# Kernel tuning notes

Measured on AMD Instinct MI355X. Metric: run time of the kernel, lower is better.

## Reference

```python
import math
import jax, jax.numpy as jnp
import numpy as np

B, S, DM, H, KH = 2, 2048, 1024, 16, 4
HD = DM // H          # 64
N_REP = H // KH       # 4
ROPE_THETA = 10000.0


def setup_inputs() -> dict:
    key = jax.random.key(0)
    ks = jax.random.split(key, 5)
    x = jax.random.normal(ks[0], (B, S, DM), dtype=jnp.float32)
    wq = jax.random.normal(ks[1], (H * HD, DM), dtype=jnp.float32) * 0.02
    wk = jax.random.normal(ks[2], (KH * HD, DM), dtype=jnp.float32) * 0.02
    wv = jax.random.normal(ks[3], (KH * HD, DM), dtype=jnp.float32) * 0.02
    wo = jax.random.normal(ks[4], (DM, H * HD), dtype=jnp.float32) * 0.02
    # freqs_cis = exp(i * t * theta^(-2j/d)) represented as cos/sin, shape [S, HD//2]
    inv_freq = 1.0 / (ROPE_THETA ** (jnp.arange(0, HD, 2, dtype=jnp.float32) / HD))
    angles = jnp.arange(S, dtype=jnp.float32)[:, None] * inv_freq[None, :]
    return {
        'x': x, 'wq': wq, 'wk': wk, 'wv': wv, 'wo': wo,
        'freqs_cos': jnp.cos(angles), 'freqs_sin': jnp.sin(angles),
    }


def _rope(t, cos, sin):
    # t: [B, S, h, HD]; pairs (even, odd) rotated as complex mul
    tr = t.reshape(*t.shape[:-1], HD // 2, 2)
    xr, xi = tr[..., 0], tr[..., 1]
    c = cos[None, :, None, :]  # [1, S, 1, HD//2]
    s = sin[None, :, None, :]
    out = jnp.stack([xr * c - xi * s, xr * s + xi * c], axis=-1)
    return out.reshape(t.shape)


def reference(x, wq, wk, wv, wo, freqs_cos, freqs_sin):
    b, s, _ = x.shape
    xq = (x @ wq.T).reshape(b, s, H, HD)
    xk = (x @ wk.T).reshape(b, s, KH, HD)
    xv = (x @ wv.T).reshape(b, s, KH, HD)
    xq = _rope(xq, freqs_cos, freqs_sin)
    xk = _rope(xk, freqs_cos, freqs_sin)
    # [B, h, S, HD]
    xq = xq.transpose(0, 2, 1, 3)
    xk = xk.transpose(0, 2, 1, 3)
    xv = xv.transpose(0, 2, 1, 3)
    # GQA: repeat_interleave kv heads to match query heads
    xk = jnp.repeat(xk, N_REP, axis=1)
    xv = jnp.repeat(xv, N_REP, axis=1)
    scale = 1.0 / math.sqrt(HD)
    scores = jnp.einsum('bhqd,bhkd->bhqk', xq, xk) * scale
    causal = jnp.tril(jnp.ones((s, s), dtype=bool))
    scores = jnp.where(causal[None, None], scores, jnp.finfo(scores.dtype).min)
    attn = jax.nn.softmax(scores, axis=-1)
    out = jnp.einsum('bhqk,bhkd->bhqd', attn, xv)
    out = out.transpose(0, 2, 1, 3).reshape(b, s, H * HD)
    return out @ wo.T
```

## Files before the change

### kernel.cpp

```cpp
#include <hip/hip_runtime.h>
#include <hip/hip_bf16.h>
#include <type_traits>

#define B_ 2
#define S_ 2048
#define DM_ 1024
#define H_ 16
#define KH_ 4
#define HD_ 64
#define NREP_ 4
#define QKV_LD 1536
#define CLOG 0.1803368801111244f
#define FIXM 8.0f

typedef float f32x4 __attribute__((ext_vector_type(4)));
typedef float f32x16 __attribute__((ext_vector_type(16)));
typedef short s16x8 __attribute__((ext_vector_type(8)));
typedef unsigned int u32x2 __attribute__((ext_vector_type(2)));

static __device__ __forceinline__ float bf2f(unsigned short u) {
  union { unsigned int u; float f; } x; x.u = ((unsigned int)u) << 16; return x.f;
}
static __device__ __forceinline__ unsigned short f2bf(float f) {
  union { float f; unsigned int u; } x; x.f = f;
  unsigned int r = (x.u + 0x7fffu + ((x.u >> 16) & 1u)) >> 16;
  return (unsigned short)r;
}
static __device__ __forceinline__ unsigned int cvtpk_bf16(float lo, float hi) {
  unsigned int r;
  asm("v_cvt_pk_bf16_f32 %0, %1, %2" : "=v"(r) : "v"(lo), "v"(hi));
  return r;
}
static __device__ __forceinline__ float fexp2(float x) {
  float r;
  asm("v_exp_f32 %0, %1" : "=v"(r) : "v"(x));
  return r;
}

__device__ __forceinline__ void gload_lds16(const unsigned short* g, unsigned short* l) {
  __builtin_amdgcn_global_load_lds(
      (const __attribute__((address_space(1))) unsigned int*)g,
      (__attribute__((address_space(3))) unsigned int*)l, 16, 0, 0);
}

__global__ void cvt_all_k(const float* __restrict__ x,
                          const float* __restrict__ wq, const float* __restrict__ wk,
                          const float* __restrict__ wv, const float* __restrict__ wo,
                          unsigned short* __restrict__ xb,
                          unsigned short* __restrict__ wqkv, unsigned short* __restrict__ wob) {
  int i = (blockIdx.x * 256 + threadIdx.x) * 4;
  const float* src; unsigned short* dst; int off;
  if (i < 4194304)      { src = x;  dst = xb;              off = i; }
  else if (i < 5242880) { src = wq; dst = wqkv;            off = i - 4194304; }
  else if (i < 5505024) { src = wk; dst = wqkv + 1048576;  off = i - 5242880; }
  else if (i < 5767168) { src = wv; dst = wqkv + 1310720;  off = i - 5505024; }
  else                  { src = wo; dst = wob;             off = i - 5767168; }
  float4 v = *(const float4*)(src + off);
  ushort4 o;
  o.x = f2bf(v.x); o.y = f2bf(v.y); o.z = f2bf(v.z); o.w = f2bf(v.w);
  *(ushort4*)(dst + off) = o;
}

#define BM 128
#define BN 128
#define BK 32

template <typename OT>
__global__ __launch_bounds__(512) void gemm_bt(const unsigned short* __restrict__ A,
                                               const unsigned short* __restrict__ Bw,
                                               OT* __restrict__ C,
                                               int M, int N, int K) {
  __shared__ unsigned short lds_a[BM * BK];
  __shared__ unsigned short lds_b[BN * BK];
  const int tid = threadIdx.x;
  const int wave = tid >> 6, lane = tid & 63;
  const int lr = lane & 15, lg = lane >> 4;
  const int m0 = blockIdx.y * BM, n0 = blockIdx.x * BN;
  const int wr = wave >> 2, wc = wave & 3;

  f32x4 acc[4][2] = {};

  const int srow = tid >> 2, scol = (tid & 3) << 3;

  for (int k0 = 0; k0 < K; k0 += BK) {
    gload_lds16(A + (size_t)(m0 + srow) * K + k0 + scol, &lds_a[tid * 8]);
    gload_lds16(Bw + (size_t)(n0 + srow) * K + k0 + scol, &lds_b[tid * 8]);
    __syncthreads();
    s16x8 af[4], bfr[2];
    #pragma unroll
    for (int mi = 0; mi < 4; ++mi)
      af[mi] = *(const s16x8*)&lds_a[(wr * 64 + mi * 16 + lr) * BK + lg * 8];
    #pragma unroll
    for (int ni = 0; ni < 2; ++ni)
      bfr[ni] = *(const s16x8*)&lds_b[(wc * 32 + ni * 16 + lr) * BK + lg * 8];
    #pragma unroll
    for (int mi = 0; mi < 4; ++mi) {
      #pragma unroll
      for (int ni = 0; ni < 2; ++ni)
        acc[mi][ni] = __builtin_amdgcn_mfma_f32_16x16x32_bf16(af[mi], bfr[ni], acc[mi][ni], 0, 0, 0);
    }
    __syncthreads();
  }
  #pragma unroll
  for (int mi = 0; mi < 4; ++mi) {
    #pragma unroll
    for (int ni = 0; ni < 2; ++ni) {
      #pragma unroll
      for (int r = 0; r < 4; ++r) {
        int row = m0 + wr * 64 + mi * 16 + lg * 4 + r;
        int col = n0 + wc * 32 + ni * 16 + lr;
        if constexpr (std::is_same<OT, unsigned short>::value)
          C[(size_t)row * N + col] = f2bf(acc[mi][ni][r]);
        else
          C[(size_t)row * N + col] = acc[mi][ni][r];
      }
    }
  }
}

__global__ void kvpack_k(const unsigned short* __restrict__ qkv,
                         const float* __restrict__ fc, const float* __restrict__ fs,
                         unsigned short* __restrict__ kp, unsigned short* __restrict__ vp) {
  int idx = blockIdx.x * 256 + threadIdx.x;
  int lane = idx & 63;
  int f  = (idx >> 6) & 3;
  int t  = (idx >> 8) & 63;
  int p  = idx >> 14;
  int b = p >> 2, kh = p & 3;
  int ql = lane & 31, hi = lane >> 5;
  {
    int s = t * 32 + ql;
    int d0 = f * 16 + hi * 8;
    const unsigned short* src = qkv + (size_t)(b * S_ + s) * QKV_LD + 1024 + kh * HD_ + d0;
    s16x8 v = *(const s16x8*)src;
    int i0 = d0 >> 1;
    float4 c4 = *(const float4*)(fc + s * 32 + i0);
    float4 s4 = *(const float4*)(fs + s * 32 + i0);
    float cc[4] = {c4.x, c4.y, c4.z, c4.w};
    float ss[4] = {s4.x, s4.y, s4.z, s4.w};
    union { s16x8 v; unsigned int w[4]; } o;
    #pragma unroll
    for (int e = 0; e < 4; ++e) {
      float xr = bf2f((unsigned short)v[2 * e]);
      float xi = bf2f((unsigned short)v[2 * e + 1]);
      o.w[e] = cvtpk_bf16(xr * cc[e] - xi * ss[e], xr * ss[e] + xi * cc[e]);
    }
    *(s16x8*)(kp + (size_t)idx * 8) = o.v;
  }
  {
    int d = (f >> 1) * 32 + ql;
    int kv0 = t * 32 + (f & 1) * 16 + hi * 8;
    const unsigned short* src = qkv + (size_t)(b * S_ + kv0) * QKV_LD + 1280 + kh * HD_ + d;
    s16x8 o;
    #pragma unroll
    for (int e = 0; e < 8; ++e) o[e] = (short)src[(size_t)e * QKV_LD];
    *(s16x8*)(vp + (size_t)idx * 8) = o;
  }
}

__global__ __launch_bounds__(256, 3) void attn_fwd10(const unsigned short* __restrict__ qkv,
                                                     const unsigned short* __restrict__ kp,
                                                     const unsigned short* __restrict__ vp,
                                                     const float* __restrict__ fc,
                                                     const float* __restrict__ fs,
                                                     unsigned short* __restrict__ ob) {
  __shared__ float mbuf[2][64][34];
  const int tid = threadIdx.x;
  const int wave = tid >> 6, lane = tid & 63;
  const int ql = lane & 31;
  const int hi = lane >> 5;
  const int bi = blockIdx.x;
  const int xcd = bi & 7;
  const int b = xcd >> 2, kh = xcd & 3;
  const int j = bi >> 3;
  const int h = kh * NREP_ + (j & 3);
  const int bt = j >> 2;

  int c, t0, t1;
  int sW1buf = -1, sM1buf = -1;
  bool sW2 = false, sM2 = false, doOut;
  if (bt < 32) {
    c = 63 - bt;
    int T = c + 1;
    t0 = (wave * T) >> 2; t1 = ((wave + 1) * T) >> 2;
    sW1buf = (wave == 1) ? 0 : (wave == 3) ? 1 : -1;
    sM1buf = (wave == 0) ? 0 : (wave == 2) ? 1 : -1;
    sW2 = (wave == 2); sM2 = (wave == 0);
    doOut = (wave == 0);
  } else if (bt < 40) {
    int bb2 = bt - 32;
    c = (wave < 2) ? (16 + bb2) : (31 - bb2);
    int T = c + 1, Th = T >> 1;
    if ((wave & 1) == 0) { t0 = 0;  t1 = Th; } else { t0 = Th; t1 = T; }
    sW1buf = (wave == 1) ? 0 : (wave == 3) ? 1 : -1;
    sM1buf = (wave == 0) ? 0 : (wave == 2) ? 1 : -1;
    doOut = (wave == 0) || (wave == 2);
  } else {
    c = (bt - 40) * 4 + wave;
    t0 = 0; t1 = c + 1;
    doOut = true;
  }
  const int q = c * 32 + ql;

  const unsigned short* qrow = qkv + (size_t)(b * S_ + q) * QKV_LD + h * HD_;
  s16x8 qf[4];
  #pragma unroll
  for (int ks = 0; ks < 4; ++ks) {
    s16x8 v = *(const s16x8*)(qrow + ks * 16 + hi * 8);
    int i0 = ks * 8 + hi * 4;
    float4 c4 = *(const float4*)(fc + q * 32 + i0);
    float4 s4 = *(const float4*)(fs + q * 32 + i0);
    float cc[4] = {c4.x, c4.y, c4.z, c4.w};
    float ss[4] = {s4.x, s4.y, s4.z, s4.w};
    union { s16x8 v; unsigned int w[4]; } o;
    #pragma unroll
    for (int e = 0; e < 4; ++e) {
      float xr = bf2f((unsigned short)v[2 * e]);
      float xi = bf2f((unsigned short)v[2 * e + 1]);
      o.w[e] = cvtpk_bf16(xr * cc[e] - xi * ss[e], xr * ss[e] + xi * cc[e]);
    }
    qf[ks] = o.v;
  }

  const unsigned short* kpt = kp + ((size_t)(b * KH_ + kh) << 17) + lane * 8;
  const unsigned short* vpt = vp + ((size_t)(b * KH_ + kh) << 17) + lane * 8;

  f32x16 oT0 = {};
  f32x16 oT1 = {};
  float l = 0.f;

  s16x8 ka[4], va[4], kb2[4], vb2[4];

#define LOADKV(T, KK, VV) do { \
    const unsigned short* kp_ = kpt + ((size_t)(T) << 11); \
    KK[0] = *(const s16x8*)(kp_);        KK[1] = *(const s16x8*)(kp_ + 512); \
    KK[2] = *(const s16x8*)(kp_ + 1024); KK[3] = *(const s16x8*)(kp_ + 1536); \
    const unsigned short* vp_ = vpt + ((size_t)(T) << 11); \
    VV[0] = *(const s16x8*)(vp_);        VV[1] = *(const s16x8*)(vp_ + 512); \
    VV[2] = *(const s16x8*)(vp_ + 1024); VV[3] = *(const s16x8*)(vp_ + 1536); \
  } while (0)

  auto body = [&](s16x8 (&KK)[4], s16x8 (&VV)[4], bool diag) __attribute__((always_inline)) {
    f32x16 st = {};
    __builtin_amdgcn_s_setprio(1);
    st = __builtin_amdgcn_mfma_f32_32x32x16_bf16(KK[0], qf[0], st, 0, 0, 0);
    st = __builtin_amdgcn_mfma_f32_32x32x16_bf16(KK[1], qf[1], st, 0, 0, 0);
    st = __builtin_amdgcn_mfma_f32_32x32x16_bf16(KK[2], qf[2], st, 0, 0, 0);
    st = __builtin_amdgcn_mfma_f32_32x32x16_bf16(KK[3], qf[3], st, 0, 0, 0);
    __builtin_amdgcn_s_setprio(0);
    if (diag) {
      #pragma unroll
      for (int r = 0; r < 16; ++r)
        if (((r & 3) + 8 * (r >> 2) + 4 * hi) > ql) st[r] = -1e30f;
    }
    float pr[16];
    #pragma unroll
    for (int r = 0; r < 16; ++r) pr[r] = fexp2(fmaf(st[r], CLOG, -FIXM));
    float s0 = (pr[0] + pr[1]) + (pr[2] + pr[3]);
    float s1 = (pr[4] + pr[5]) + (pr[6] + pr[7]);
    float s2 = (pr[8] + pr[9]) + (pr[10] + pr[11]);
    float s3 = (pr[12] + pr[13]) + (pr[14] + pr[15]);
    l += (s0 + s1) + (s2 + s3);
    #pragma unroll
    for (int ksv = 0; ksv < 2; ++ksv) {
      unsigned int a01 = cvtpk_bf16(pr[ksv * 8 + 0], pr[ksv * 8 + 1]);
      unsigned int a23 = cvtpk_bf16(pr[ksv * 8 + 2], pr[ksv * 8 + 3]);
      unsigned int b45 = cvtpk_bf16(pr[ksv * 8 + 4], pr[ksv * 8 + 5]);
      unsigned int b67 = cvtpk_bf16(pr[ksv * 8 + 6], pr[ksv * 8 + 7]);
      asm volatile("v_permlane32_swap_b32 %0, %1" : "+v"(a01), "+v"(b45));
      asm volatile("v_permlane32_swap_b32 %0, %1" : "+v"(a23), "+v"(b67));
      union { s16x8 v; unsigned int w[4]; } pb;
      pb.w[0] = a01; pb.w[1] = a23; pb.w[2] = b45; pb.w[3] = b67;
      __builtin_amdgcn_s_setprio(1);
      oT0 = __builtin_amdgcn_mfma_f32_32x32x16_bf16(VV[ksv], pb.v, oT0, 0, 0, 0);
      oT1 = __builtin_amdgcn_mfma_f32_32x32x16_bf16(VV[2 + ksv], pb.v, oT1, 0, 0, 0);
      __builtin_amdgcn_s_setprio(0);
    }
  };

  LOADKV(t0, ka, va);
  int t = t0;
  while (t + 1 < t1) {
    LOADKV(t + 1, kb2, vb2);
    body(ka, va, t == c);
    ++t;
    if (t + 1 < t1) LOADKV(t + 1, ka, va);
    body(kb2, vb2, t == c);
    ++t;
  }
  if (t < t1) body(ka, va, t == c);
#undef LOADKV

#define WRITEP(BUF) do { float* mp_ = &mbuf[BUF][lane][0]; \
    _Pragma("unroll") for (int r = 0; r < 16; ++r) { mp_[r] = oT0[r]; mp_[16 + r] = oT1[r]; } \
    mp_[32] = l; } while (0)
#define MERGEP(BUF) do { float* mp_ = &mbuf[BUF][lane][0]; \
    l += mp_[32]; \
    _Pragma("unroll") for (int r = 0; r < 16; ++r) { \
      oT0[r] += mp_[r]; \
      oT1[r] += mp_[16 + r]; } } while (0)

  __syncthreads();
  if (sW1buf >= 0) WRITEP(sW1buf);
  __syncthreads();
  if (sM1buf >= 0) MERGEP(sM1buf);
  __syncthreads();
  if (sW2) WRITEP(0);
  __syncthreads();
  if (sM2) MERGEP(0);
#undef WRITEP
#undef MERGEP

  if (doOut) {
    float l_tot = l + __shfl_xor(l, 32);
    float invl = 1.0f / l_tot;
    unsigned short* orow = ob + (size_t)(b * S_ + q) * DM_ + h * HD_;
    #pragma unroll
    for (int dblk = 0; dblk < 2; ++dblk) {
      #pragma unroll
      for (int g = 0; g < 4; ++g) {
        float e0 = (dblk ? oT1[4 * g + 0] : oT0[4 * g + 0]) * invl;
        float e1 = (dblk ? oT1[4 * g + 1] : oT0[4 * g + 1]) * invl;
        float e2 = (dblk ? oT1[4 * g + 2] : oT0[4 * g + 2]) * invl;
        float e3 = (dblk ? oT1[4 * g + 3] : oT0[4 * g + 3]) * invl;
        u32x2 w;
        w.x = cvtpk_bf16(e0, e1);
        w.y = cvtpk_bf16(e2, e3);
        *(u32x2*)(orow + dblk * 32 + g * 8 + 4 * hi) = w;
      }
    }
  }
}

extern "C" void kernel_launch(void* const* d_in, const int* in_sizes, int n_in,
                              void* d_out, int out_size, void* d_ws, size_t ws_size,
                              hipStream_t stream) {
  const float* x  = (const float*)d_in[0];
  const float* wq = (const float*)d_in[1];
  const float* wk = (const float*)d_in[2];
  const float* wv = (const float*)d_in[3];
  const float* wo = (const float*)d_in[4];
  const float* fc = (const float*)d_in[5];
  const float* fs = (const float*)d_in[6];
  float* out = (float*)d_out;

  const size_t nX    = (size_t)B_ * S_ * DM_;
  const size_t nWQKV = (size_t)QKV_LD * DM_;
  const size_t nWO   = (size_t)DM_ * DM_;
  const size_t nQKV  = (size_t)B_ * S_ * QKV_LD;
  const size_t nKV   = (size_t)B_ * S_ * KH_ * HD_;

  unsigned short* xb    = (unsigned short*)d_ws;
  unsigned short* wqkv  = xb + nX;
  unsigned short* wob   = wqkv + nWQKV;
  unsigned short* qkv   = wob + nWO;
  unsigned short* kpk   = qkv + nQKV;
  unsigned short* vpk   = kpk + nKV;
  unsigned short* a_buf = vpk + nKV;

  const int M = B_ * S_;

  cvt_all_k<<<6656, 256, 0, stream>>>(x, wq, wk, wv, wo, xb, wqkv, wob);

  gemm_bt<unsigned short><<<dim3(QKV_LD / BN, M / BM), 512, 0, stream>>>(
      xb, wqkv, qkv, M, QKV_LD, DM_);

  kvpack_k<<<512, 256, 0, stream>>>(qkv, fc, fs, kpk, vpk);

  attn_fwd10<<<1408, 256, 0, stream>>>(qkv, kpk, vpk, fc, fs, a_buf);

  gemm_bt<float><<<dim3(DM_ / BN, M / BM), 512, 0, stream>>>(
      a_buf, wob, out, M, DM_, DM_);
}
```

Baseline: 98.92 us.

## Double GEMM K-tile, remap blocks per XCD, split QK MFMA chains

The GEMM K-step doubles from 32 to 64, which halves the number of barrier-synchronized iterations, and the LDS tiles grow to match. Blocks are now launched on a 1D grid and remapped so that consecutive tiles land on the same XCD, aiming for better L2 reuse. In attention, the four dependent QK^T MFMAs are split into two independent accumulators that are summed afterward, and the causal mask is folded into the exp loop to shorten the dependency chain. The costs are more LDS use per GEMM block and a few extra adds per score element.

```diff
diff --git a/kernel.cpp b/kernel.cpp
--- a/kernel.cpp
+++ b/kernel.cpp
@@ -63,41 +63,48 @@
 
 #define BM 128
 #define BN 128
-#define BK 32
 
 template <typename OT>
 __global__ __launch_bounds__(512) void gemm_bt(const unsigned short* __restrict__ A,
                                                const unsigned short* __restrict__ Bw,
                                                OT* __restrict__ C,
                                                int M, int N, int K) {
-  __shared__ unsigned short lds_a[BM * BK];
-  __shared__ unsigned short lds_b[BN * BK];
+  __shared__ unsigned short lds_a[BM * 64];
+  __shared__ unsigned short lds_b[BN * 64];
   const int tid = threadIdx.x;
   const int wave = tid >> 6, lane = tid & 63;
   const int lr = lane & 15, lg = lane >> 4;
-  const int m0 = blockIdx.y * BM, n0 = blockIdx.x * BN;
+  const int nbx = N / BN;
+  const int cpx = gridDim.x >> 3;
+  const int bid = blockIdx.x;
+  const int wg = (bid & 7) * cpx + (bid >> 3);
+  const int m0 = (wg / nbx) * BM, n0 = (wg % nbx) * BN;
   const int wr = wave >> 2, wc = wave & 3;
 
   f32x4 acc[4][2] = {};
-
-  const int srow = tid >> 2, scol = (tid & 3) << 3;
-
-  for (int k0 = 0; k0 < K; k0 += BK) {
+  const int srow = tid >> 3, scol = (tid & 7) << 3;
+
+  for (int k0 = 0; k0 < K; k0 += 64) {
     gload_lds16(A + (size_t)(m0 + srow) * K + k0 + scol, &lds_a[tid * 8]);
+    gload_lds16(A + (size_t)(m0 + 64 + srow) * K + k0 + scol, &lds_a[4096 + tid * 8]);
     gload_lds16(Bw + (size_t)(n0 + srow) * K + k0 + scol, &lds_b[tid * 8]);
+    gload_lds16(Bw + (size_t)(n0 + 64 + srow) * K + k0 + scol, &lds_b[4096 + tid * 8]);
     __syncthreads();
-    s16x8 af[4], bfr[2];
-    #pragma unroll
-    for (int mi = 0; mi < 4; ++mi)
-      af[mi] = *(const s16x8*)&lds_a[(wr * 64 + mi * 16 + lr) * BK + lg * 8];
-    #pragma unroll
-    for (int ni = 0; ni < 2; ++ni)
-      bfr[ni] = *(const s16x8*)&lds_b[(wc * 32 + ni * 16 + lr) * BK + lg * 8];
-    #pragma unroll
-    for (int mi = 0; mi < 4; ++mi) {
+    #pragma unroll
+    for (int kk = 0; kk < 2; ++kk) {
+      s16x8 af[4], bfr[2];
+      #pragma unroll
+      for (int mi = 0; mi < 4; ++mi)
+        af[mi] = *(const s16x8*)&lds_a[(wr * 64 + mi * 16 + lr) * 64 + kk * 32 + lg * 8];
       #pragma unroll
       for (int ni = 0; ni < 2; ++ni)
-        acc[mi][ni] = __builtin_amdgcn_mfma_f32_16x16x32_bf16(af[mi], bfr[ni], acc[mi][ni], 0, 0, 0);
+        bfr[ni] = *(const s16x8*)&lds_b[(wc * 32 + ni * 16 + lr) * 64 + kk * 32 + lg * 8];
+      #pragma unroll
+      for (int mi = 0; mi < 4; ++mi) {
+        #pragma unroll
+        for (int ni = 0; ni < 2; ++ni)
+          acc[mi][ni] = __builtin_amdgcn_mfma_f32_16x16x32_bf16(af[mi], bfr[ni], acc[mi][ni], 0, 0, 0);
+      }
     }
     __syncthreads();
   }
@@ -158,7 +165,7 @@
   }
 }
 
-__global__ __launch_bounds__(256, 3) void attn_fwd10(const unsigned short* __restrict__ qkv,
+__global__ __launch_bounds__(256, 3) void attn_fwd11(const unsigned short* __restrict__ qkv,
                                                      const unsigned short* __restrict__ kp,
                                                      const unsigned short* __restrict__ vp,
                                                      const float* __restrict__ fc,
@@ -241,21 +248,20 @@
   } while (0)
 
   auto body = [&](s16x8 (&KK)[4], s16x8 (&VV)[4], bool diag) __attribute__((always_inline)) {
-    f32x16 st = {};
+    f32x16 stA = {}, stB = {};
     __builtin_amdgcn_s_setprio(1);
-    st = __builtin_amdgcn_mfma_f32_32x32x16_bf16(KK[0], qf[0], st, 0, 0, 0);
-    st = __builtin_amdgcn_mfma_f32_32x32x16_bf16(KK[1], qf[1], st, 0, 0, 0);
-    st = __builtin_amdgcn_mfma_f32_32x32x16_bf16(KK[2], qf[2], st, 0, 0, 0);
-    st = __builtin_amdgcn_mfma_f32_32x32x16_bf16(KK[3], qf[3], st, 0, 0, 0);
+    stA = __builtin_amdgcn_mfma_f32_32x32x16_bf16(KK[0], qf[0], stA, 0, 0, 0);
+    stB = __builtin_amdgcn_mfma_f32_32x32x16_bf16(KK[2], qf[2], stB, 0, 0, 0);
+    stA = __builtin_amdgcn_mfma_f32_32x32x16_bf16(KK[1], qf[1], stA, 0, 0, 0);
+    stB = __builtin_amdgcn_mfma_f32_32x32x16_bf16(KK[3], qf[3], stB, 0, 0, 0);
     __builtin_amdgcn_s_setprio(0);
-    if (diag) {
-      #pragma unroll
-      for (int r = 0; r < 16; ++r)
-        if (((r & 3) + 8 * (r >> 2) + 4 * hi) > ql) st[r] = -1e30f;
-    }
     float pr[16];
     #pragma unroll
-    for (int r = 0; r < 16; ++r) pr[r] = fexp2(fmaf(st[r], CLOG, -FIXM));
+    for (int r = 0; r < 16; ++r) {
+      float sv = stA[r] + stB[r];
+      if (diag && (((r & 3) + 8 * (r >> 2) + 4 * hi) > ql)) sv = -1e30f;
+      pr[r] = fexp2(fmaf(sv, CLOG, -FIXM));
+    }
     float s0 = (pr[0] + pr[1]) + (pr[2] + pr[3]);
     float s1 = (pr[4] + pr[5]) + (pr[6] + pr[7]);
     float s2 = (pr[8] + pr[9]) + (pr[10] + pr[11]);
@@ -362,13 +368,13 @@
 
   cvt_all_k<<<6656, 256, 0, stream>>>(x, wq, wk, wv, wo, xb, wqkv, wob);
 
-  gemm_bt<unsigned short><<<dim3(QKV_LD / BN, M / BM), 512, 0, stream>>>(
+  gemm_bt<unsigned short><<<(QKV_LD / BN) * (M / BM), 512, 0, stream>>>(
       xb, wqkv, qkv, M, QKV_LD, DM_);
 
   kvpack_k<<<512, 256, 0, stream>>>(qkv, fc, fs, kpk, vpk);
 
-  attn_fwd10<<<1408, 256, 0, stream>>>(qkv, kpk, vpk, fc, fs, a_buf);
-
-  gemm_bt<float><<<dim3(DM_ / BN, M / BM), 512, 0, stream>>>(
+  attn_fwd11<<<1408, 256, 0, stream>>>(qkv, kpk, vpk, fc, fs, a_buf);
+
+  gemm_bt<float><<<(DM_ / BN) * (M / BM), 512, 0, stream>>>(
       a_buf, wob, out, M, DM_, DM_);
 }
```

Result: slower. 105.0 us (+6.2%).
